# Optimization experiments

Hardware: AMD Instinct MI355X
Metric: run time of the kernel (lower is better)

Reference implementation:

```python
import jax, jax.numpy as jnp
import numpy as np

B, T, D, H = 128, 512, 16, 512


def lstm_layer(x, h0, c0, Wih, Whh, b):
    """Single LSTM layer, batch_first input x: (B,T,Din). Torch gate order i,f,g,o.
    b is the sum of torch's b_ih + b_hh (identical math)."""
    def step(carry, xt):
        h, c = carry
        gates = xt @ Wih.T + h @ Whh.T + b  # (B, 4H)
        i, f, g, o = jnp.split(gates, 4, axis=-1)
        i = jax.nn.sigmoid(i)
        f = jax.nn.sigmoid(f)
        g = jnp.tanh(g)
        o = jax.nn.sigmoid(o)
        c = f * c + i * g
        h = o * jnp.tanh(c)
        return (h, c), h

    (hT, cT), ys = jax.lax.scan(step, (h0, c0), jnp.swapaxes(x, 0, 1))
    return jnp.swapaxes(ys, 0, 1), hT, cT  # (B,T,H), (B,H), (B,H)


def setup_inputs() -> dict:
    key = jax.random.key(0)
    ks = jax.random.split(key, 16)
    s = 1.0 / np.sqrt(H)  # torch LSTM/Linear init scale
    u = lambda k, shape: jax.random.uniform(k, shape, jnp.float32, -s, s)
    return {
        "x": jax.random.normal(ks[0], (B, T, D), jnp.float32),
        # encoder layer 0: input_dim -> H ; layer 1: H -> H
        "enc_Wih0": u(ks[1], (4 * H, D)),
        "enc_Whh0": u(ks[2], (4 * H, H)),
        "enc_b0": u(ks[3], (4 * H,)),
        "enc_Wih1": u(ks[4], (4 * H, H)),
        "enc_Whh1": u(ks[5], (4 * H, H)),
        "enc_b1": u(ks[6], (4 * H,)),
        # decoder layers: H -> H
        "dec_Wih0": u(ks[7], (4 * H, H)),
        "dec_Whh0": u(ks[8], (4 * H, H)),
        "dec_b0": u(ks[9], (4 * H,)),
        "dec_Wih1": u(ks[10], (4 * H, H)),
        "dec_Whh1": u(ks[11], (4 * H, H)),
        "dec_b1": u(ks[12], (4 * H,)),
        # output projection H -> D
        "W_out": u(ks[13], (D, H)),
        "b_out": u(ks[14], (D,)),
    }


def reference(x, enc_Wih0, enc_Whh0, enc_b0, enc_Wih1, enc_Whh1, enc_b1,
              dec_Wih0, dec_Whh0, dec_b0, dec_Wih1, dec_Whh1, dec_b1,
              W_out, b_out):
    z = jnp.zeros((x.shape[0], H), x.dtype)
    # encoder (2 stacked layers, eval mode -> no dropout)
    y0, h0, c0 = lstm_layer(x, z, z, enc_Wih0, enc_Whh0, enc_b0)
    y1, h1, c1 = lstm_layer(y0, z, z, enc_Wih1, enc_Whh1, enc_b1)
    encoding = h1  # h_n[-1]
    # decoder input: encoding repeated across time
    dec_in = jnp.broadcast_to(encoding[:, None, :], (x.shape[0], x.shape[1], H))
    # decoder initial state = encoder final (h_n, c_n), per-layer
    d0, _, _ = lstm_layer(dec_in, h0, c0, dec_Wih0, dec_Whh0, dec_b0)
    d1, _, _ = lstm_layer(d0, h1, c1, dec_Wih1, dec_Whh1, dec_b1)
    reconstructed = d1 @ W_out.T + b_out  # (B,T,D)
    return reconstructed, encoding
```

## Files before the change

### kernel.cpp

```cpp
#include <hip/hip_runtime.h>
#include <math.h>


#define NB 128
#define NT 512
#define ND 16
#define NH 512
#define NWG 256
#define NTHR 256
#define NGRP 8
#define GWG 32

typedef __attribute__((ext_vector_type(8))) short short8;
typedef __attribute__((ext_vector_type(4))) float float4v;
typedef __attribute__((ext_vector_type(4))) unsigned int uint4v;

#define SCOPE_AGT __HIP_MEMORY_SCOPE_AGENT

#define BAR_BYTES 16384
#define PLANE_BYTES (NB * NH * 4)
#define CHUNK_BYTES (32 * NB * 4)
#define AH_PLANE(wsB, L, par) ((wsB) + BAR_BYTES + (size_t)((L) * 2 + (par)) * PLANE_BYTES)
#define H3F_PTR(wsB, par) ((float*)((wsB) + BAR_BYTES + 8 * (size_t)PLANE_BYTES + (size_t)(par) * NB * NH * 4))

__device__ __forceinline__ void st_u32_agt(unsigned* p, unsigned v) {
  __hip_atomic_store(p, v, __ATOMIC_RELAXED, SCOPE_AGT);
}
__device__ __forceinline__ unsigned ld_u32_agt(const unsigned* p) {
  return __hip_atomic_load(p, __ATOMIC_RELAXED, SCOPE_AGT);
}

__device__ __forceinline__ void loadpair(const char* pa, const char* pb,
                                         uint4v (&d)[4]) {
  asm volatile(
      "global_load_dwordx4 %0, %4, off sc1\n\t"
      "global_load_dwordx4 %1, %4, off offset:16 sc1\n\t"
      "global_load_dwordx4 %2, %5, off sc1\n\t"
      "global_load_dwordx4 %3, %5, off offset:16 sc1\n\t"
      "s_waitcnt vmcnt(0)"
      : "=&v"(d[0]), "=&v"(d[1]), "=&v"(d[2]), "=&v"(d[3])
      : "v"(pa), "v"(pb)
      : "memory");
}

__device__ __forceinline__ void gbar(unsigned* flags, int hb, unsigned& epoch) {
  ++epoch;
  __syncthreads();
  if (threadIdx.x < 64) {
    if (threadIdx.x == 0) st_u32_agt(flags + hb, epoch);
    const unsigned* fp = flags + (threadIdx.x & 31);
    for (;;) {
      unsigned v = ld_u32_agt(fp);
      if (__all((int)(v - epoch) >= 0)) break;
      __builtin_amdgcn_s_sleep(1);
    }
  }
  __syncthreads();
}

__device__ __forceinline__ unsigned short f2bf(float f) {
  union { float f; unsigned u; } v; v.f = f;
  unsigned r = v.u + 0x7fffu + ((v.u >> 16) & 1u);
  return (unsigned short)(r >> 16);
}
__device__ __forceinline__ float bf2f(unsigned short u) {
  union { float f; unsigned u; } v; v.u = ((unsigned)u) << 16; return v.f;
}
__device__ __forceinline__ void split2(float f, unsigned short& hi, unsigned short& lo) {
  hi = f2bf(f);
  lo = f2bf(f - bf2f(hi));
}
__device__ __forceinline__ void load_wfrag(const float* __restrict__ p, short8& h, short8& l) {
#pragma unroll
  for (int j = 0; j < 8; ++j) {
    unsigned short a, b2; split2(p[j], a, b2);
    h[j] = (short)a; l[j] = (short)b2;
  }
}
__device__ __forceinline__ void load_frags_single(const float* __restrict__ W, int w, int hb, int lane,
                                                  short8 (&fh)[4][4], short8 (&fl)[4][4]) {
  const int ln = lane & 15, lq = lane >> 4;
#pragma unroll
  for (int cc = 0; cc < 4; ++cc) {
    const int k = (w * 4 + cc) * 32 + lq * 8;
#pragma unroll
    for (int g = 0; g < 4; ++g)
      load_wfrag(W + (size_t)(g * NH + hb * 16 + ln) * NH + k, fh[cc][g], fl[cc][g]);
  }
}
__device__ __forceinline__ void load_frags_concat(const float* __restrict__ Wa, const float* __restrict__ Wb,
                                                  int w, int hb, int lane,
                                                  short8 (&fh)[8][4], short8 (&fl)[8][4]) {
  const int ln = lane & 15, lq = lane >> 4;
#pragma unroll
  for (int cc = 0; cc < 8; ++cc) {
    const int k = (w * 8 + cc) * 32 + lq * 8;
    const float* W = (k < 512) ? Wa : Wb;
    const int kk = (k < 512) ? k : k - 512;
#pragma unroll
    for (int g = 0; g < 4; ++g)
      load_wfrag(W + (size_t)(g * NH + hb * 16 + ln) * NH + kk, fh[cc][g], fl[cc][g]);
  }
}

__device__ __forceinline__ void consume2(const uint4v& a, const uint4v& b,
                                         const short8 (&wh)[4], const short8 (&wl)[4],
                                         float4v (&acc)[4]) {
  unsigned x0 = a[0], x1 = a[1], x2 = a[2], x3 = a[3];
  unsigned x4 = b[0], x5 = b[1], x6 = b[2], x7 = b[3];
  union U { unsigned u[4]; short8 s; } A, L;
  A.u[0] = (x0 & 0xffffu) | (x1 << 16);
  A.u[1] = (x2 & 0xffffu) | (x3 << 16);
  A.u[2] = (x4 & 0xffffu) | (x5 << 16);
  A.u[3] = (x6 & 0xffffu) | (x7 << 16);
  L.u[0] = (x0 >> 16) | (x1 & 0xffff0000u);
  L.u[1] = (x2 >> 16) | (x3 & 0xffff0000u);
  L.u[2] = (x4 >> 16) | (x5 & 0xffff0000u);
  L.u[3] = (x6 >> 16) | (x7 & 0xffff0000u);
  const short8 ah = A.s, al = L.s;
#pragma unroll
  for (int g = 0; g < 4; ++g) {
    acc[g] = __builtin_amdgcn_mfma_f32_16x16x32_bf16(ah, wh[g], acc[g], 0, 0, 0);
    acc[g] = __builtin_amdgcn_mfma_f32_16x16x32_bf16(ah, wl[g], acc[g], 0, 0, 0);
    acc[g] = __builtin_amdgcn_mfma_f32_16x16x32_bf16(al, wh[g], acc[g], 0, 0, 0);
  }
}
__device__ __forceinline__ void write_red(float* __restrict__ red, int w, int lane, const float4v (&acc)[4]) {
  const int ln = lane & 15, lq = lane >> 4;
#pragma unroll
  for (int g = 0; g < 4; ++g)
#pragma unroll
    for (int r = 0; r < 4; ++r)
      red[((w * 4 + g) * 16 + (lq * 4 + r)) * 16 + ln] = acc[g][r];
}
__device__ __forceinline__ void store_h(char* __restrict__ plane, int b, int hid, float h) {
  unsigned short hi, lo; split2(h, hi, lo);
  const size_t off = (size_t)(hid >> 5) * CHUNK_BYTES + (size_t)b * 128 + (size_t)(hid & 31) * 4;
  unsigned v = (unsigned)hi | ((unsigned)lo << 16);
  st_u32_agt((unsigned*)(plane + off), v);
}
__device__ __forceinline__ float sigf(float v) { return 1.f / (1.f + __expf(-v)); }

extern "C" __global__ __launch_bounds__(NTHR, 1)
void lstm_ae_kernel(const float* __restrict__ x,
                    const float* __restrict__ eWih0, const float* __restrict__ eWhh0, const float* __restrict__ eb0,
                    const float* __restrict__ eWih1, const float* __restrict__ eWhh1, const float* __restrict__ eb1,
                    const float* __restrict__ dWih0, const float* __restrict__ dWhh0, const float* __restrict__ db0,
                    const float* __restrict__ dWih1, const float* __restrict__ dWhh1, const float* __restrict__ db1,
                    const float* __restrict__ Wout,  const float* __restrict__ bout,
                    float* __restrict__ out, char* __restrict__ wsB) {
  __shared__ float red0[4 * 4 * 16 * 16];
  __shared__ float red1[4 * 4 * 16 * 16];

  const int tid = threadIdx.x;
  const int lane = tid & 63;
  const int w = tid >> 6;

  const int grp = (int)(blockIdx.x & 7u);
  const int hb  = (int)(blockIdx.x >> 3);

  unsigned* flags = (unsigned*)(wsB + (size_t)grp * 1024);
  unsigned epoch = 0;

  const int b0 = grp * 16;
  const int ln = lane & 15, lq = lane >> 4;
  const int aoff = (b0 + ln) * 128 + lq * 32;
  const int bi = tid >> 4, hi_ = tid & 15;
  const int b = b0 + bi, hid = hb * 16 + hi_;
  const float4v zacc = {0.f, 0.f, 0.f, 0.f};

  store_h(AH_PLANE(wsB, 0, 1), b, hid, 0.f);
  store_h(AH_PLANE(wsB, 1, 1), b, hid, 0.f);
  float c0 = 0.f, c1 = 0.f, c2 = 0.f, c3 = 0.f;
  const float eb0v[4] = {eb0[hid], eb0[NH + hid], eb0[2 * NH + hid], eb0[3 * NH + hid]};
  const float eb1v[4] = {eb1[hid], eb1[NH + hid], eb1[2 * NH + hid], eb1[3 * NH + hid]};
  const float db1v[4] = {db1[hid], db1[NH + hid], db1[2 * NH + hid], db1[3 * NH + hid]};

  short8 w0h[4][4], w0l[4][4];
  short8 w1h[8][4], w1l[8][4];
  load_frags_single(eWhh0, w, hb, lane, w0h, w0l);
  load_frags_concat(eWih1, eWhh1, w, hb, lane, w1h, w1l);
  gbar(flags, hb, epoch);

  float h0fin = 0.f, h1fin = 0.f;

  for (int i = 0; i <= NT; ++i) {
    const int pw = i & 1, pr = pw ^ 1;
    const int te = i - 1;
    const int pA = te & 1, pB = pA ^ 1;
    const char* p0 = AH_PLANE(wsB, 0, pr);
    const char* p1 = (w < 2) ? AH_PLANE(wsB, 0, pA) : AH_PLANE(wsB, 1, pB);
    const int c1i = (w < 2) ? w * 8 : (w - 2) * 8;
    float4v acc0[4] = {zacc, zacc, zacc, zacc};
    float4v acc1[4] = {zacc, zacc, zacc, zacc};
    uint4v d[4];

    loadpair(p0 + (size_t)(w * 4 + 0) * CHUNK_BYTES + aoff,
             p0 + (size_t)(w * 4 + 1) * CHUNK_BYTES + aoff, d);
    consume2(d[0], d[1], w0h[0], w0l[0], acc0);
    consume2(d[2], d[3], w0h[1], w0l[1], acc0);
    loadpair(p0 + (size_t)(w * 4 + 2) * CHUNK_BYTES + aoff,
             p0 + (size_t)(w * 4 + 3) * CHUNK_BYTES + aoff, d);
    consume2(d[0], d[1], w0h[2], w0l[2], acc0);
    consume2(d[2], d[3], w0h[3], w0l[3], acc0);
    write_red(red0, w, lane, acc0);
#pragma unroll
    for (int pp = 0; pp < 4; ++pp) {
      loadpair(p1 + (size_t)(c1i + 2 * pp) * CHUNK_BYTES + aoff,
               p1 + (size_t)(c1i + 2 * pp + 1) * CHUNK_BYTES + aoff, d);
      consume2(d[0], d[1], w1h[2 * pp], w1l[2 * pp], acc1);
      consume2(d[2], d[3], w1h[2 * pp + 1], w1l[2 * pp + 1], acc1);
    }
    write_red(red1, w, lane, acc1);
    __syncthreads();

    if (i < NT) {
      float s[4];
#pragma unroll
      for (int g = 0; g < 4; ++g) {
        float v = eb0v[g];
#pragma unroll
        for (int ww = 0; ww < 4; ++ww) v += red0[((ww * 4 + g) * 16 + bi) * 16 + hi_];
        s[g] = v;
      }
      const float* xr = x + ((size_t)b * NT + i) * ND;
      float xv[16];
#pragma unroll
      for (int j = 0; j < 16; ++j) xv[j] = xr[j];
#pragma unroll
      for (int g = 0; g < 4; ++g) {
        const float* wr = eWih0 + (size_t)(g * NH + hid) * ND;
        float v = 0.f;
#pragma unroll
        for (int j = 0; j < 16; ++j) v += xv[j] * wr[j];
        s[g] += v;
      }
      float ig = sigf(s[0]), fg = sigf(s[1]), gg = tanhf(s[2]), og = sigf(s[3]);
      c0 = fg * c0 + ig * gg;
      float h = og * tanhf(c0);
      store_h(AH_PLANE(wsB, 0, pw), b, hid, h);
      if (i == NT - 1) h0fin = h;
    }
    if (i >= 1) {
      float s[4];
#pragma unroll
      for (int g = 0; g < 4; ++g) {
        float v = eb1v[g];
#pragma unroll
        for (int ww = 0; ww < 4; ++ww) v += red1[((ww * 4 + g) * 16 + bi) * 16 + hi_];
        s[g] = v;
      }
      float ig = sigf(s[0]), fg = sigf(s[1]), gg = tanhf(s[2]), og = sigf(s[3]);
      c1 = fg * c1 + ig * gg;
      float h = og * tanhf(c1);
      store_h(AH_PLANE(wsB, 1, pA), b, hid, h);
      if (te == NT - 1) h1fin = h;
    }
    gbar(flags, hb, epoch);
  }

  out[(size_t)NB * NT * ND + (size_t)b * NH + hid] = h1fin;
  c2 = c0; c3 = c1;
  store_h(AH_PLANE(wsB, 2, 1), b, hid, h0fin);
  store_h(AH_PLANE(wsB, 3, 1), b, hid, h1fin);

  float Gbreg[4];
  load_frags_single(dWih0, w, hb, lane, w0h, w0l);
  {
    const char* ph = AH_PLANE(wsB, 1, 1);
    float4v acc[4] = {zacc, zacc, zacc, zacc};
    uint4v d[4];
    loadpair(ph + (size_t)(w * 4 + 0) * CHUNK_BYTES + aoff,
             ph + (size_t)(w * 4 + 1) * CHUNK_BYTES + aoff, d);
    consume2(d[0], d[1], w0h[0], w0l[0], acc);
    consume2(d[2], d[3], w0h[1], w0l[1], acc);
    loadpair(ph + (size_t)(w * 4 + 2) * CHUNK_BYTES + aoff,
             ph + (size_t)(w * 4 + 3) * CHUNK_BYTES + aoff, d);
    consume2(d[0], d[1], w0h[2], w0l[2], acc);
    consume2(d[2], d[3], w0h[3], w0l[3], acc);
    write_red(red0, w, lane, acc);
    __syncthreads();
#pragma unroll
    for (int g = 0; g < 4; ++g) {
      float v = db0[g * NH + hid];
#pragma unroll
      for (int ww = 0; ww < 4; ++ww) v += red0[((ww * 4 + g) * 16 + bi) * 16 + hi_];
      Gbreg[g] = v;
    }
  }
  load_frags_single(dWhh0, w, hb, lane, w0h, w0l);
  load_frags_concat(dWih1, dWhh1, w, hb, lane, w1h, w1l);
  gbar(flags, hb, epoch);

  const int idxA = hb * 8 + w * 2, idxB = idxA + 1;
  const int pbA = b0 + (idxA >> 4), pdA = idxA & 15;
  const int pbB = b0 + (idxB >> 4), pdB = idxB & 15;

  for (int i = 0; i <= NT + 1; ++i) {
    const int pw = i & 1, pr = pw ^ 1;
    const int te = i - 1, tp = i - 2;
    const int pA = te & 1, pB = pA ^ 1;
    const char* p0 = AH_PLANE(wsB, 2, pr);
    const char* p1 = (w < 2) ? AH_PLANE(wsB, 2, pA) : AH_PLANE(wsB, 3, pB);
    const int c1i = (w < 2) ? w * 8 : (w - 2) * 8;
    const float* H3 = H3F_PTR(wsB, tp & 1);
    float4v acc0[4] = {zacc, zacc, zacc, zacc};
    float4v acc1[4] = {zacc, zacc, zacc, zacc};
    uint4v d[4];

    loadpair(p0 + (size_t)(w * 4 + 0) * CHUNK_BYTES + aoff,
             p0 + (size_t)(w * 4 + 1) * CHUNK_BYTES + aoff, d);
    consume2(d[0], d[1], w0h[0], w0l[0], acc0);
    consume2(d[2], d[3], w0h[1], w0l[1], acc0);
    loadpair(p0 + (size_t)(w * 4 + 2) * CHUNK_BYTES + aoff,
             p0 + (size_t)(w * 4 + 3) * CHUNK_BYTES + aoff, d);
    consume2(d[0], d[1], w0h[2], w0l[2], acc0);
    consume2(d[2], d[3], w0h[3], w0l[3], acc0);
    write_red(red0, w, lane, acc0);
#pragma unroll
    for (int pp = 0; pp < 4; ++pp) {
      loadpair(p1 + (size_t)(c1i + 2 * pp) * CHUNK_BYTES + aoff,
               p1 + (size_t)(c1i + 2 * pp + 1) * CHUNK_BYTES + aoff, d);
      consume2(d[0], d[1], w1h[2 * pp], w1l[2 * pp], acc1);
      consume2(d[2], d[3], w1h[2 * pp + 1], w1l[2 * pp + 1], acc1);
    }
    write_red(red1, w, lane, acc1);
    uint4v dp[4];
    loadpair((const char*)(H3 + (size_t)pbA * NH) + (size_t)lane * 32,
             (const char*)(H3 + (size_t)pbB * NH) + (size_t)lane * 32, dp);
    __syncthreads();

    if (i >= 2) {
#pragma unroll
      for (int rep = 0; rep < 2; ++rep) {
        union PU { uint4v u; float f[4]; } u0, u1;
        u0.u = dp[2 * rep]; u1.u = dp[2 * rep + 1];
        const int pd = rep ? pdB : pdA;
        const float* wr = Wout + (size_t)pd * NH + lane * 8;
        float ssum = u0.f[0] * wr[0] + u0.f[1] * wr[1] + u0.f[2] * wr[2] + u0.f[3] * wr[3]
                   + u1.f[0] * wr[4] + u1.f[1] * wr[5] + u1.f[2] * wr[6] + u1.f[3] * wr[7];
#pragma unroll
        for (int off = 32; off >= 1; off >>= 1) ssum += __shfl_xor(ssum, off, 64);
        if (lane == 0)
          out[((size_t)(rep ? pbB : pbA) * NT + tp) * ND + pd] = ssum + bout[pd];
      }
    }
    if (i < NT) {
      float s[4];
#pragma unroll
      for (int g = 0; g < 4; ++g) {
        float v = Gbreg[g];
#pragma unroll
        for (int ww = 0; ww < 4; ++ww) v += red0[((ww * 4 + g) * 16 + bi) * 16 + hi_];
        s[g] = v;
      }
      float ig = sigf(s[0]), fg = sigf(s[1]), gg = tanhf(s[2]), og = sigf(s[3]);
      c2 = fg * c2 + ig * gg;
      float h = og * tanhf(c2);
      store_h(AH_PLANE(wsB, 2, pw), b, hid, h);
    }
    if (i >= 1 && i <= NT) {
      float s[4];
#pragma unroll
      for (int g = 0; g < 4; ++g) {
        float v = db1v[g];
#pragma unroll
        for (int ww = 0; ww < 4; ++ww) v += red1[((ww * 4 + g) * 16 + bi) * 16 + hi_];
        s[g] = v;
      }
      float ig = sigf(s[0]), fg = sigf(s[1]), gg = tanhf(s[2]), og = sigf(s[3]);
      c3 = fg * c3 + ig * gg;
      float h = og * tanhf(c3);
      store_h(AH_PLANE(wsB, 3, pA), b, hid, h);
      __hip_atomic_store(H3F_PTR(wsB, pA) + (size_t)b * NH + hid, h,
                         __ATOMIC_RELAXED, SCOPE_AGT);
    }
    if (i != NT + 1) gbar(flags, hb, epoch);
  }
}

extern "C" void kernel_launch(void* const* d_in, const int* in_sizes, int n_in,
                              void* d_out, int out_size, void* d_ws, size_t ws_size,
                              hipStream_t stream) {
  const float* xp    = (const float*)d_in[0];
  const float* eWih0 = (const float*)d_in[1];
  const float* eWhh0 = (const float*)d_in[2];
  const float* eb0   = (const float*)d_in[3];
  const float* eWih1 = (const float*)d_in[4];
  const float* eWhh1 = (const float*)d_in[5];
  const float* eb1   = (const float*)d_in[6];
  const float* dWih0 = (const float*)d_in[7];
  const float* dWhh0 = (const float*)d_in[8];
  const float* db0   = (const float*)d_in[9];
  const float* dWih1 = (const float*)d_in[10];
  const float* dWhh1 = (const float*)d_in[11];
  const float* db1   = (const float*)d_in[12];
  const float* Wout  = (const float*)d_in[13];
  const float* bout  = (const float*)d_in[14];

  hipMemsetAsync(d_ws, 0, BAR_BYTES, stream);
  lstm_ae_kernel<<<NWG, NTHR, 0, stream>>>(
      xp, eWih0, eWhh0, eb0, eWih1, eWhh1, eb1,
      dWih0, dWhh0, db0, dWih1, dWhh1, db1, Wout, bout,
      (float*)d_out, (char*)d_ws);
}
```

Baseline: 9.218 ms.

## Stage recurrent state chunks via global_load_lds with single wait per step

Replaces the serialized inline-asm register load pairs (each followed by a full vmcnt wait) with direct global-to-LDS loads that issue all 12 state chunks for both layers up front. A single wait then precedes MFMA consumption from LDS. The goal is to cut the per-step memory latency that sits on the recurrent critical path. Other loads now use relaxed agent-scope 64-bit atomic loads instead of the sc1 asm. The change adds 96KB of LDS plus extra LDS reads, and the coherence of the LDS-path loads (aux bits 17) is uncertain.

```diff
diff --git a/kernel.cpp b/kernel.cpp
--- a/kernel.cpp
+++ b/kernel.cpp
@@ -9,7 +9,6 @@
 #define NWG 256
 #define NTHR 256
 #define NGRP 8
-#define GWG 32
 
 typedef __attribute__((ext_vector_type(8))) short short8;
 typedef __attribute__((ext_vector_type(4))) float float4v;
@@ -29,18 +28,34 @@
 __device__ __forceinline__ unsigned ld_u32_agt(const unsigned* p) {
   return __hip_atomic_load(p, __ATOMIC_RELAXED, SCOPE_AGT);
 }
-
-__device__ __forceinline__ void loadpair(const char* pa, const char* pb,
-                                         uint4v (&d)[4]) {
-  asm volatile(
-      "global_load_dwordx4 %0, %4, off sc1\n\t"
-      "global_load_dwordx4 %1, %4, off offset:16 sc1\n\t"
-      "global_load_dwordx4 %2, %5, off sc1\n\t"
-      "global_load_dwordx4 %3, %5, off offset:16 sc1\n\t"
-      "s_waitcnt vmcnt(0)"
-      : "=&v"(d[0]), "=&v"(d[1]), "=&v"(d[2]), "=&v"(d[3])
-      : "v"(pa), "v"(pb)
-      : "memory");
+__device__ __forceinline__ unsigned long long ld_u64_agt(const void* p) {
+  return __hip_atomic_load((const unsigned long long*)p, __ATOMIC_RELAXED, SCOPE_AGT);
+}
+
+__device__ __forceinline__ void gload_lds(const char* g, char* l) {
+  __builtin_amdgcn_global_load_lds(
+      (const __attribute__((address_space(1))) unsigned int*)g,
+      (__attribute__((address_space(3))) unsigned int*)l, 16, 0, 17);
+}
+__device__ __forceinline__ void stage_chunk(const char* g, char* slot) {
+  gload_lds(g, slot);
+  gload_lds(g + 16, slot + 1024);
+}
+
+__device__ __forceinline__ void loadpair_at(const char* pa, const char* pb,
+                                            uint4v (&d)[4]) {
+#pragma unroll
+  for (int r = 0; r < 2; ++r) {
+    const char* base = r ? pb : pa;
+    unsigned long long q0 = ld_u64_agt(base);
+    unsigned long long q1 = ld_u64_agt(base + 8);
+    unsigned long long q2 = ld_u64_agt(base + 16);
+    unsigned long long q3 = ld_u64_agt(base + 24);
+    d[2 * r][0] = (unsigned)q0; d[2 * r][1] = (unsigned)(q0 >> 32);
+    d[2 * r][2] = (unsigned)q1; d[2 * r][3] = (unsigned)(q1 >> 32);
+    d[2 * r + 1][0] = (unsigned)q2; d[2 * r + 1][1] = (unsigned)(q2 >> 32);
+    d[2 * r + 1][2] = (unsigned)q3; d[2 * r + 1][3] = (unsigned)(q3 >> 32);
+  }
 }
 
 __device__ __forceinline__ void gbar(unsigned* flags, int hb, unsigned& epoch) {
@@ -125,6 +140,13 @@
     acc[g] = __builtin_amdgcn_mfma_f32_16x16x32_bf16(al, wh[g], acc[g], 0, 0, 0);
   }
 }
+__device__ __forceinline__ void consume_lds(const char* slot, int lane,
+                                            const short8 (&wh)[4], const short8 (&wl)[4],
+                                            float4v (&acc)[4]) {
+  const uint4v a = *(const uint4v*)(slot + lane * 16);
+  const uint4v b = *(const uint4v*)(slot + 1024 + lane * 16);
+  consume2(a, b, wh, wl, acc);
+}
 __device__ __forceinline__ void write_red(float* __restrict__ red, int w, int lane, const float4v (&acc)[4]) {
   const int ln = lane & 15, lq = lane >> 4;
 #pragma unroll
@@ -151,6 +173,7 @@
                     float* __restrict__ out, char* __restrict__ wsB) {
   __shared__ float red0[4 * 4 * 16 * 16];
   __shared__ float red1[4 * 4 * 16 * 16];
+  __shared__ __attribute__((aligned(16))) char stage[4][12 * 2048];
 
   const int tid = threadIdx.x;
   const int lane = tid & 63;
@@ -168,6 +191,7 @@
   const int bi = tid >> 4, hi_ = tid & 15;
   const int b = b0 + bi, hid = hb * 16 + hi_;
   const float4v zacc = {0.f, 0.f, 0.f, 0.f};
+  char* sb = &stage[w][0];
 
   store_h(AH_PLANE(wsB, 0, 1), b, hid, 0.f);
   store_h(AH_PLANE(wsB, 1, 1), b, hid, 0.f);
@@ -193,24 +217,23 @@
     const int c1i = (w < 2) ? w * 8 : (w - 2) * 8;
     float4v acc0[4] = {zacc, zacc, zacc, zacc};
     float4v acc1[4] = {zacc, zacc, zacc, zacc};
-    uint4v d[4];
-
-    loadpair(p0 + (size_t)(w * 4 + 0) * CHUNK_BYTES + aoff,
-             p0 + (size_t)(w * 4 + 1) * CHUNK_BYTES + aoff, d);
-    consume2(d[0], d[1], w0h[0], w0l[0], acc0);
-    consume2(d[2], d[3], w0h[1], w0l[1], acc0);
-    loadpair(p0 + (size_t)(w * 4 + 2) * CHUNK_BYTES + aoff,
-             p0 + (size_t)(w * 4 + 3) * CHUNK_BYTES + aoff, d);
-    consume2(d[0], d[1], w0h[2], w0l[2], acc0);
-    consume2(d[2], d[3], w0h[3], w0l[3], acc0);
+
+#pragma unroll
+    for (int cc = 0; cc < 4; ++cc)
+      stage_chunk(p0 + (size_t)(w * 4 + cc) * CHUNK_BYTES + aoff, sb + cc * 2048);
+#pragma unroll
+    for (int cc = 0; cc < 8; ++cc)
+      stage_chunk(p1 + (size_t)(c1i + cc) * CHUNK_BYTES + aoff, sb + (4 + cc) * 2048);
+    asm volatile("s_waitcnt vmcnt(0)" ::: "memory");
+    __builtin_amdgcn_sched_barrier(0);
+
+#pragma unroll
+    for (int cc = 0; cc < 4; ++cc)
+      consume_lds(sb + cc * 2048, lane, w0h[cc], w0l[cc], acc0);
     write_red(red0, w, lane, acc0);
 #pragma unroll
-    for (int pp = 0; pp < 4; ++pp) {
-      loadpair(p1 + (size_t)(c1i + 2 * pp) * CHUNK_BYTES + aoff,
-               p1 + (size_t)(c1i + 2 * pp + 1) * CHUNK_BYTES + aoff, d);
-      consume2(d[0], d[1], w1h[2 * pp], w1l[2 * pp], acc1);
-      consume2(d[2], d[3], w1h[2 * pp + 1], w1l[2 * pp + 1], acc1);
-    }
+    for (int cc = 0; cc < 8; ++cc)
+      consume_lds(sb + (4 + cc) * 2048, lane, w1h[cc], w1l[cc], acc1);
     write_red(red1, w, lane, acc1);
     __syncthreads();
 
@@ -270,12 +293,12 @@
     const char* ph = AH_PLANE(wsB, 1, 1);
     float4v acc[4] = {zacc, zacc, zacc, zacc};
     uint4v d[4];
-    loadpair(ph + (size_t)(w * 4 + 0) * CHUNK_BYTES + aoff,
-             ph + (size_t)(w * 4 + 1) * CHUNK_BYTES + aoff, d);
+    loadpair_at(ph + (size_t)(w * 4 + 0) * CHUNK_BYTES + aoff,
+                ph + (size_t)(w * 4 + 1) * CHUNK_BYTES + aoff, d);
     consume2(d[0], d[1], w0h[0], w0l[0], acc);
     consume2(d[2], d[3], w0h[1], w0l[1], acc);
-    loadpair(ph + (size_t)(w * 4 + 2) * CHUNK_BYTES + aoff,
-             ph + (size_t)(w * 4 + 3) * CHUNK_BYTES + aoff, d);
+    loadpair_at(ph + (size_t)(w * 4 + 2) * CHUNK_BYTES + aoff,
+                ph + (size_t)(w * 4 + 3) * CHUNK_BYTES + aoff, d);
     consume2(d[0], d[1], w0h[2], w0l[2], acc);
     consume2(d[2], d[3], w0h[3], w0l[3], acc);
     write_red(red0, w, lane, acc);
@@ -306,28 +329,27 @@
     const float* H3 = H3F_PTR(wsB, tp & 1);
     float4v acc0[4] = {zacc, zacc, zacc, zacc};
     float4v acc1[4] = {zacc, zacc, zacc, zacc};
-    uint4v d[4];
-
-    loadpair(p0 + (size_t)(w * 4 + 0) * CHUNK_BYTES + aoff,
-             p0 + (size_t)(w * 4 + 1) * CHUNK_BYTES + aoff, d);
-    consume2(d[0], d[1], w0h[0], w0l[0], acc0);
-    consume2(d[2], d[3], w0h[1], w0l[1], acc0);
-    loadpair(p0 + (size_t)(w * 4 + 2) * CHUNK_BYTES + aoff,
-             p0 + (size_t)(w * 4 + 3) * CHUNK_BYTES + aoff, d);
-    consume2(d[0], d[1], w0h[2], w0l[2], acc0);
-    consume2(d[2], d[3], w0h[3], w0l[3], acc0);
+
+#pragma unroll
+    for (int cc = 0; cc < 4; ++cc)
+      stage_chunk(p0 + (size_t)(w * 4 + cc) * CHUNK_BYTES + aoff, sb + cc * 2048);
+#pragma unroll
+    for (int cc = 0; cc < 8; ++cc)
+      stage_chunk(p1 + (size_t)(c1i + cc) * CHUNK_BYTES + aoff, sb + (4 + cc) * 2048);
+    asm volatile("s_waitcnt vmcnt(0)" ::: "memory");
+    __builtin_amdgcn_sched_barrier(0);
+
+#pragma unroll
+    for (int cc = 0; cc < 4; ++cc)
+      consume_lds(sb + cc * 2048, lane, w0h[cc], w0l[cc], acc0);
     write_red(red0, w, lane, acc0);
 #pragma unroll
-    for (int pp = 0; pp < 4; ++pp) {
-      loadpair(p1 + (size_t)(c1i + 2 * pp) * CHUNK_BYTES + aoff,
-               p1 + (size_t)(c1i + 2 * pp + 1) * CHUNK_BYTES + aoff, d);
-      consume2(d[0], d[1], w1h[2 * pp], w1l[2 * pp], acc1);
-      consume2(d[2], d[3], w1h[2 * pp + 1], w1l[2 * pp + 1], acc1);
-    }
+    for (int cc = 0; cc < 8; ++cc)
+      consume_lds(sb + (4 + cc) * 2048, lane, w1h[cc], w1l[cc], acc1);
     write_red(red1, w, lane, acc1);
     uint4v dp[4];
-    loadpair((const char*)(H3 + (size_t)pbA * NH) + (size_t)lane * 32,
-             (const char*)(H3 + (size_t)pbB * NH) + (size_t)lane * 32, dp);
+    loadpair_at((const char*)(H3 + (size_t)pbA * NH) + (size_t)lane * 32,
+                (const char*)(H3 + (size_t)pbB * NH) + (size_t)lane * 32, dp);
     __syncthreads();
 
     if (i >= 2) {
```

New measurement: 10.70 ms. 16.0% more time.
